# Optimization experiments

Hardware: AMD Instinct MI355X
Metric: run time of the kernel (lower is better)

## Reference

```python
import jax, jax.numpy as jnp
import numpy as np

ROPE_BASE = 10000.0

def apply_rope(x):
    # x: [B, S, H, Dh]  (rotate-half / NeoX convention)
    B, S, H, Dh = x.shape
    inv_freq = 1.0 / (ROPE_BASE ** (jnp.arange(0, Dh, 2, dtype=jnp.float32) / Dh))  # [Dh/2]
    ang = jnp.arange(S, dtype=jnp.float32)[:, None] * inv_freq[None, :]             # [S, Dh/2]
    cos = jnp.cos(ang)[None, :, None, :].astype(x.dtype)  # [1,S,1,Dh/2]
    sin = jnp.sin(ang)[None, :, None, :].astype(x.dtype)
    x1, x2 = jnp.split(x, 2, axis=-1)
    return jnp.concatenate([x1 * cos - x2 * sin, x1 * sin + x2 * cos], axis=-1)

def setup_inputs() -> dict:
    key = jax.random.key(0)
    k1, k2, k3 = jax.random.split(key, 3)
    B, S, D = 2, 2048, 1024
    x = jax.random.normal(k1, (B, S, D), dtype=jnp.float32)
    attn_mask = jnp.ones((B, S), dtype=bool)
    qkv_w = jax.random.normal(k2, (D, 3 * D), dtype=jnp.float32) * (1.0 / np.sqrt(D))
    out_w = jax.random.normal(k3, (D, D), dtype=jnp.float32) * (1.0 / np.sqrt(D))
    return {"x": x, "qkv_w": qkv_w, "out_w": out_w, "attn_mask": attn_mask, "is_causal": 1}

def reference(x, qkv_w, out_w, attn_mask, is_causal):
    B, S, D = x.shape
    H = 16
    Dh = D // H
    qkv = x @ qkv_w                                  # [B,S,3D]
    q, k, v = jnp.split(qkv, 3, axis=-1)
    q = apply_rope(q.reshape(B, S, H, Dh))           # [B,S,H,Dh]
    k = apply_rope(k.reshape(B, S, H, Dh))
    v = v.reshape(B, S, H, Dh)
    scale = 1.0 / np.sqrt(Dh)
    att = jnp.einsum('bqhd,bkhd->bhqk', q, k) * scale  # [B,H,S,S]
    if is_causal:
        mask = jnp.tril(jnp.ones((S, S), dtype=bool))[None, None]
    else:
        mask = attn_mask[:, None, None, :]             # [B,1,1,S]
    att = jnp.where(mask, att, jnp.finfo(att.dtype).min)
    p = jax.nn.softmax(att, axis=-1)
    y = jnp.einsum('bhqk,bkhd->bqhd', p, v).reshape(B, S, D)
    return y @ out_w
```

## Files before the change

kernel.cpp:

```cpp
#include <hip/hip_runtime.h>
#include <hip/hip_bf16.h>

#define BB 2
#define SS 2048
#define DD 1024
#define HH 16
#define N3 3072

#define POH (32 * 16 * 64 * 64)
#define PLH (32 * 16 * 64)

typedef __attribute__((ext_vector_type(8))) short bf16x8;
typedef __attribute__((ext_vector_type(4))) float f32x4;
typedef __attribute__((ext_vector_type(2))) unsigned int u32x2;

__device__ __forceinline__ float b2f(unsigned short u) {
    return __uint_as_float(((unsigned int)u) << 16);
}
__device__ __forceinline__ unsigned short f2b(float f) {
    unsigned int x = __float_as_uint(f);
    x += 0x7fffu + ((x >> 16) & 1u);
    return (unsigned short)(x >> 16);
}
__device__ __forceinline__ unsigned int pack2bf(float a, float b) {
    __hip_bfloat162 h = __float22bfloat162_rn(make_float2(a, b));
    return *(unsigned int*)&h;
}
__device__ __forceinline__ void storeC(float* p, float v) { *p = v; }
__device__ __forceinline__ void storeC(unsigned short* p, float v) { *p = f2b(v); }

__device__ __forceinline__ void gload_lds16(const void* g, void* l) {
    __builtin_amdgcn_global_load_lds(
        (__attribute__((address_space(1))) void*)g,
        (__attribute__((address_space(3))) void*)l, 16, 0, 0);
}

__global__ __launch_bounds__(256) void sincos_tab(float2* __restrict__ tab) {
    int i = blockIdx.x * 256 + threadIdx.x;
    int t = i & 31;
    int s = i >> 5;
    float inv = powf(10000.0f, -(float)t * (1.0f / 32.0f));
    float sn, c;
    sincosf((float)s * inv, &sn, &c);
    tab[i] = make_float2(c, sn);
}

__global__ __launch_bounds__(256) void cast_f32_bf16(
    const float* __restrict__ src, unsigned short* __restrict__ dst)
{
    int i = (blockIdx.x * 256 + threadIdx.x) * 4;
    float4 f = *(const float4*)(src + i);
    uint2 o;
    o.x = pack2bf(f.x, f.y);
    o.y = pack2bf(f.z, f.w);
    *(uint2*)(dst + i) = o;
}

__global__ __launch_bounds__(256) void cast_transpose(
    const float* __restrict__ src, unsigned short* __restrict__ dst,
    int R, int C)
{
    __shared__ unsigned short tile[64][66];
    const int t = threadIdx.x;
    const int c0 = blockIdx.x * 64, r0 = blockIdx.y * 64;
    const int lr = t >> 4;
    const int lc = (t & 15) * 4;
    #pragma unroll
    for (int i = 0; i < 4; ++i) {
        float4 f = *(const float4*)(src + (size_t)(r0 + lr + i * 16) * C + c0 + lc);
        tile[lr + i * 16][lc + 0] = f2b(f.x);
        tile[lr + i * 16][lc + 1] = f2b(f.y);
        tile[lr + i * 16][lc + 2] = f2b(f.z);
        tile[lr + i * 16][lc + 3] = f2b(f.w);
    }
    __syncthreads();
    #pragma unroll
    for (int i = 0; i < 4; ++i) {
        const int wr = lr + i * 16;
        ushort4 o;
        o.x = tile[lc + 0][wr];
        o.y = tile[lc + 1][wr];
        o.z = tile[lc + 2][wr];
        o.w = tile[lc + 3][wr];
        *(ushort4*)(dst + (size_t)(c0 + wr) * R + r0 + lc) = o;
    }
}

template <typename OutT, int TN>
__global__ __launch_bounds__(256) void gemm_mfma(
    const unsigned short* __restrict__ A,
    const unsigned short* __restrict__ Bt,
    OutT* __restrict__ C,
    int M, int N, int K)
{
    constexpr int NI = TN / 32;
    constexpr int NB = TN / 64;
    __shared__ unsigned short Al[128 * 32];
    __shared__ unsigned short Bl[TN * 32];
    const int tid  = threadIdx.x;
    const int wave = tid >> 6;
    const int lane = tid & 63;
    const int quad = lane >> 4;
    const int l16  = lane & 15;
    const int m0 = blockIdx.y * 128;
    const int n0 = blockIdx.x * TN;
    const int wm = (wave >> 1) * 64;
    const int wn = (wave & 1) * (TN / 2);

    const int srowA = wave * 32 + (lane >> 2);
    const int srowB = wave * (16 * NB) + (lane >> 2);
    const int scol  = (lane & 3) * 8;
    const unsigned short* gA = A  + (size_t)(m0 + srowA) * K + scol;
    const unsigned short* gB = Bt + (size_t)(n0 + srowB) * K + scol;

    f32x4 acc[4][NI];
    #pragma unroll
    for (int mi = 0; mi < 4; ++mi)
        #pragma unroll
        for (int ni = 0; ni < NI; ++ni)
            acc[mi][ni] = (f32x4){0.f, 0.f, 0.f, 0.f};

    for (int k0 = 0; k0 < K; k0 += 32) {
        __syncthreads();
        #pragma unroll
        for (int i = 0; i < 2; ++i)
            gload_lds16(gA + (size_t)i * 16 * K + k0, Al + (wave * 2 + i) * 512);
        #pragma unroll
        for (int i = 0; i < NB; ++i)
            gload_lds16(gB + (size_t)i * 16 * K + k0, Bl + (wave * NB + i) * 512);
        __syncthreads();

        bf16x8 af[4], bfr[NI];
        #pragma unroll
        for (int mi = 0; mi < 4; ++mi)
            af[mi] = *(const bf16x8*)&Al[(wm + mi * 16 + l16) * 32 + quad * 8];
        #pragma unroll
        for (int ni = 0; ni < NI; ++ni)
            bfr[ni] = *(const bf16x8*)&Bl[(wn + ni * 16 + l16) * 32 + quad * 8];
        #pragma unroll
        for (int mi = 0; mi < 4; ++mi)
            #pragma unroll
            for (int ni = 0; ni < NI; ++ni)
                acc[mi][ni] = __builtin_amdgcn_mfma_f32_16x16x32_bf16(
                    af[mi], bfr[ni], acc[mi][ni], 0, 0, 0);
    }

    #pragma unroll
    for (int mi = 0; mi < 4; ++mi) {
        #pragma unroll
        for (int r = 0; r < 4; ++r) {
            const size_t base = (size_t)(m0 + wm + mi * 16 + quad * 4 + r) * N + n0 + wn;
            #pragma unroll
            for (int ni = 0; ni < NI; ++ni)
                storeC(&C[base + ni * 16 + l16], acc[mi][ni][r]);
        }
    }
}

__global__ __launch_bounds__(256) void rope_split(
    const unsigned short* __restrict__ qkv,
    const float2* __restrict__ tab,
    unsigned short* __restrict__ qo,
    unsigned short* __restrict__ ko,
    unsigned short* __restrict__ vt)
{
    __shared__ unsigned short Vtile[64][72];

    const float SC = 0.18033688011112042f;
    const int s0 = blockIdx.x * 64;
    const int h  = blockIdx.y;
    const int b  = blockIdx.z;
    const int tid = threadIdx.x;
    const int sl = tid >> 2;
    const int qu = tid & 3;
    const size_t bh = (size_t)b * HH + h;

    const unsigned short* row = qkv + (size_t)(b * SS + s0 + sl) * N3 + h * 64;

    uint4 a0 = *(const uint4*)(row + qu * 8);
    uint4 a1 = *(const uint4*)(row + 32 + qu * 8);
    uint4 b0 = *(const uint4*)(row + DD + qu * 8);
    uint4 b1 = *(const uint4*)(row + DD + 32 + qu * 8);
    uint4 c0 = *(const uint4*)(row + 2 * DD + qu * 8);
    uint4 c1 = *(const uint4*)(row + 2 * DD + 32 + qu * 8);

    float2 cs[8];
    {
        const float4* tp = (const float4*)(tab + (size_t)(s0 + sl) * 32 + qu * 8);
        #pragma unroll
        for (int i = 0; i < 4; ++i) {
            float4 f = tp[i];
            cs[2 * i]     = make_float2(f.x, f.y);
            cs[2 * i + 1] = make_float2(f.z, f.w);
        }
    }

    const unsigned short* pa0 = (const unsigned short*)&a0;
    const unsigned short* pa1 = (const unsigned short*)&a1;
    const unsigned short* pb0 = (const unsigned short*)&b0;
    const unsigned short* pb1 = (const unsigned short*)&b1;
    const unsigned short* pc0 = (const unsigned short*)&c0;
    const unsigned short* pc1 = (const unsigned short*)&c1;

    unsigned short oq1[8], oq2[8], ok1[8], ok2[8];
    #pragma unroll
    for (int j = 0; j < 8; ++j) {
        float c = cs[j].x, sn = cs[j].y;
        float q1 = b2f(pa0[j]), q2 = b2f(pa1[j]);
        float k1 = b2f(pb0[j]), k2 = b2f(pb1[j]);
        oq1[j] = f2b((q1 * c - q2 * sn) * SC);
        oq2[j] = f2b((q1 * sn + q2 * c) * SC);
        ok1[j] = f2b(k1 * c - k2 * sn);
        ok2[j] = f2b(k1 * sn + k2 * c);
        Vtile[qu * 8 + j][sl]      = pc0[j];
        Vtile[32 + qu * 8 + j][sl] = pc1[j];
    }
    const size_t qoff = (bh * SS + s0 + sl) * 64;
    *(uint4*)(qo + qoff + qu * 8)      = *(const uint4*)oq1;
    *(uint4*)(qo + qoff + 32 + qu * 8) = *(const uint4*)oq2;
    *(uint4*)(ko + qoff + qu * 8)      = *(const uint4*)ok1;
    *(uint4*)(ko + qoff + 32 + qu * 8) = *(const uint4*)ok2;

    __syncthreads();

    const int dr = tid >> 2;
    const int ch = tid & 3;
    uint4 t0 = *(const uint4*)&Vtile[dr][ch * 16];
    uint4 t1 = *(const uint4*)&Vtile[dr][ch * 16 + 8];
    unsigned short* vrow = vt + (bh * 64 + dr) * SS + s0 + ch * 16;
    *(uint4*)vrow       = t0;
    *(uint4*)(vrow + 8) = t1;
}

__device__ __forceinline__ void attn_step(
    const unsigned short* __restrict__ Kb,
    const unsigned short* __restrict__ Vb,
    const bf16x8 qf0, const bf16x8 qf1, const bf16x8 onesf,
    f32x4 O[4], f32x4& l_acc,
    bool diag, const unsigned char* mrow,
    int kt, int quad, int l16, int csw, int qg)
{
    f32x4 Sf[4];
    __builtin_amdgcn_s_setprio(1);
    #pragma unroll
    for (int st = 0; st < 4; ++st) {
        const unsigned short* kr = &Kb[(st * 16 + l16) * 64];
        bf16x8 kf0 = *(const bf16x8*)(kr + csw * 8);
        bf16x8 kf1 = *(const bf16x8*)(kr + (csw ^ 4) * 8);
        f32x4 s = (f32x4){0.f, 0.f, 0.f, 0.f};
        s = __builtin_amdgcn_mfma_f32_16x16x32_bf16(kf0, qf0, s, 0, 0, 0);
        s = __builtin_amdgcn_mfma_f32_16x16x32_bf16(kf1, qf1, s, 0, 0, 0);
        Sf[st] = s;
    }
    __builtin_amdgcn_s_setprio(0);

    if (diag) {
        #pragma unroll
        for (int st = 0; st < 4; ++st) {
            const int kb0 = kt * 64 + st * 16 + quad * 4;
            #pragma unroll
            for (int r = 0; r < 4; ++r)
                if (kb0 + r > qg) Sf[st][r] = -1e30f;
        }
    } else if (mrow) {
        #pragma unroll
        for (int st = 0; st < 4; ++st) {
            uchar4 mv = *(const uchar4*)(mrow + st * 16 + quad * 4);
            if (!mv.x) Sf[st][0] = -1e30f;
            if (!mv.y) Sf[st][1] = -1e30f;
            if (!mv.z) Sf[st][2] = -1e30f;
            if (!mv.w) Sf[st][3] = -1e30f;
        }
    }

    #pragma unroll
    for (int st = 0; st < 4; ++st)
        #pragma unroll
        for (int r = 0; r < 4; ++r)
            Sf[st][r] = exp2f(Sf[st][r]);

    unsigned int W[4][2];
    #pragma unroll
    for (int st = 0; st < 4; ++st) {
        W[st][0] = pack2bf(Sf[st][0], Sf[st][1]);
        W[st][1] = pack2bf(Sf[st][2], Sf[st][3]);
    }

    unsigned int pw0[4], pw1[4];
    #pragma unroll
    for (int j = 0; j < 2; ++j) {
        u32x2 s1 = __builtin_amdgcn_permlane32_swap(W[0][j], W[1][j], false, false);
        u32x2 s2 = __builtin_amdgcn_permlane16_swap(s1.x, s1.y, false, false);
        pw0[j]     = s2.x;
        pw0[j + 2] = s2.y;
        u32x2 t1 = __builtin_amdgcn_permlane32_swap(W[2][j], W[3][j], false, false);
        u32x2 t2 = __builtin_amdgcn_permlane16_swap(t1.x, t1.y, false, false);
        pw1[j]     = t2.x;
        pw1[j + 2] = t2.y;
    }
    bf16x8 pf0 = *(const bf16x8*)pw0;
    bf16x8 pf1 = *(const bf16x8*)pw1;

    __builtin_amdgcn_s_setprio(1);
    l_acc = __builtin_amdgcn_mfma_f32_16x16x32_bf16(onesf, pf0, l_acc, 0, 0, 0);
    l_acc = __builtin_amdgcn_mfma_f32_16x16x32_bf16(onesf, pf1, l_acc, 0, 0, 0);
    #pragma unroll
    for (int st = 0; st < 4; ++st) {
        const unsigned short* vr = &Vb[(st * 16 + l16) * 64];
        bf16x8 vf0 = *(const bf16x8*)(vr + csw * 8);
        bf16x8 vf1 = *(const bf16x8*)(vr + (csw ^ 4) * 8);
        O[st] = __builtin_amdgcn_mfma_f32_16x16x32_bf16(vf0, pf0, O[st], 0, 0, 0);
        O[st] = __builtin_amdgcn_mfma_f32_16x16x32_bf16(vf1, pf1, O[st], 0, 0, 0);
    }
    __builtin_amdgcn_s_setprio(0);
}

__global__ __launch_bounds__(256) void flash_attn(
    const unsigned short* __restrict__ q,
    const unsigned short* __restrict__ k,
    const unsigned short* __restrict__ vt,
    unsigned short* __restrict__ y,
    float* __restrict__ pO,
    float* __restrict__ pL,
    const int* __restrict__ is_causal,
    const unsigned char* __restrict__ attn_mask)
{
    __shared__ unsigned short Kl[2][64 * 64];
    __shared__ unsigned short Vl[2][64 * 64];

    const int bid  = blockIdx.x;
    const int work = (bid & 7) * 192 + (bid >> 3);
    const int bhi  = work / 48;
    const int s    = work % 48;
    const int b = bhi >> 4;
    const int h = bhi & 15;
    const bool causal = (is_causal[0] != 0);

    int tile, k0t, k1t;
    bool split;
    if (s < 16) {
        tile = 16 + s; k0t = 0; k1t = 15; split = true;
    } else {
        const int r = s - 16, p = r >> 1;
        if (r & 1) { tile = 15 - p; k0t = 0;  k1t = causal ? tile : 31; split = false; }
        else       { tile = 31 - p; k0t = 16; k1t = causal ? tile : 31; split = true;  }
    }
    const int half = (s < 16) ? 0 : 1;

    const int tid  = threadIdx.x;
    const int wave = tid >> 6;
    const int lane = tid & 63;
    const int quad = lane >> 4;
    const int l16  = lane & 15;

    const size_t bh = (size_t)b * HH + h;

    const int qg = tile * 64 + wave * 16 + l16;
    const unsigned short* qrow = q + (bh * SS + qg) * 64;
    const bf16x8 qf0 = *(const bf16x8*)(qrow + quad * 8);
    const bf16x8 qf1 = *(const bf16x8*)(qrow + 32 + quad * 8);

    bf16x8 onesf;
    #pragma unroll
    for (int i = 0; i < 8; ++i) onesf[i] = (short)0x3F80;

    const unsigned short* kbase  = k  + bh * SS * 64;
    const unsigned short* vtbase = vt + bh * 64 * SS;

    const int Rl  = lane >> 3;
    const int cph = lane & 7;
    const int csw = quad ^ (l16 & 7);

    f32x4 O[4];
    #pragma unroll
    for (int st = 0; st < 4; ++st) O[st] = (f32x4){0.f, 0.f, 0.f, 0.f};
    f32x4 l_acc = (f32x4){0.f, 0.f, 0.f, 0.f};

    auto stage = [&](int kt) {
        const int buf = kt & 1;
        #pragma unroll
        for (int i = 0; i < 2; ++i) {
            const int jj = wave * 2 + i;
            const int R  = jj * 8 + Rl;
            const int cl = cph ^ (R & 7);
            gload_lds16(kbase + ((size_t)(kt * 64 + R) * 64 + cl * 8),
                        &Kl[buf][jj * 512]);
            gload_lds16(vtbase + ((size_t)R * SS + kt * 64 + cl * 8),
                        &Vl[buf][jj * 512]);
        }
    };

    stage(k0t);
    for (int kt = k0t; kt <= k1t; ++kt) {
        __syncthreads();
        if (kt + 1 <= k1t) stage(kt + 1);

        const unsigned char* mrow = causal ? nullptr
                                           : (attn_mask + (size_t)b * SS + kt * 64);
        attn_step(Kl[kt & 1], Vl[kt & 1], qf0, qf1, onesf, O, l_acc,
                  causal && kt == tile, mrow, kt, quad, l16, csw, qg);
    }

    if (!split) {
        const float inv = 1.0f / l_acc[0];
        unsigned short* yrow = y + ((size_t)b * SS + qg) * DD + h * 64;
        #pragma unroll
        for (int st = 0; st < 4; ++st) {
            uint2 o;
            o.x = pack2bf(O[st][0] * inv, O[st][1] * inv);
            o.y = pack2bf(O[st][2] * inv, O[st][3] * inv);
            *(uint2*)(yrow + st * 16 + quad * 4) = o;
        }
    } else {
        float* ob = pO + (size_t)half * POH
                  + (((bh * 16 + (size_t)(tile - 16)) * 64 + wave * 16 + l16) * 64);
        #pragma unroll
        for (int st = 0; st < 4; ++st)
            *(f32x4*)(ob + st * 16 + quad * 4) = O[st];
        if (quad == 0)
            pL[(size_t)half * PLH + (bh * 16 + (size_t)(tile - 16)) * 64
               + wave * 16 + l16] = l_acc[0];
    }
}

__global__ __launch_bounds__(256) void attn_merge(
    const float* __restrict__ pO, const float* __restrict__ pL,
    unsigned short* __restrict__ y)
{
    const int i = (blockIdx.x * 256 + threadIdx.x) * 4;
    float4 oa = *(const float4*)(pO + i);
    float4 obv = *(const float4*)(pO + POH + i);
    const int rowi = i >> 6;
    const int d    = i & 63;
    const float inv = 1.0f / (pL[rowi] + pL[PLH + rowi]);
    const int row = rowi & 63;
    const int tt  = (rowi >> 6) & 15;
    const int bh  = rowi >> 10;
    const int b = bh >> 4, h = bh & 15;
    const int sq = (16 + tt) * 64 + row;
    unsigned short* yp = y + ((size_t)b * SS + sq) * DD + h * 64 + d;
    uint2 ov;
    ov.x = pack2bf((oa.x + obv.x) * inv, (oa.y + obv.y) * inv);
    ov.y = pack2bf((oa.z + obv.z) * inv, (oa.w + obv.w) * inv);
    *(uint2*)yp = ov;
}

extern "C" void kernel_launch(void* const* d_in, const int* in_sizes, int n_in,
                              void* d_out, int out_size, void* d_ws, size_t ws_size,
                              hipStream_t stream) {
    const float* x      = (const float*)d_in[0];
    const float* qkv_w  = (const float*)d_in[1];
    const float* out_w  = (const float*)d_in[2];
    const unsigned char* mask = (const unsigned char*)d_in[3];
    const int*   is_c   = (const int*)d_in[4];
    float* out = (float*)d_out;

    unsigned short* xb  = (unsigned short*)d_ws;
    unsigned short* w1t = xb  + (size_t)4096 * 1024;
    unsigned short* w2t = w1t + (size_t)3072 * 1024;
    unsigned short* qkv = w2t + (size_t)1024 * 1024;
    unsigned short* qb  = qkv + (size_t)4096 * 3072;
    unsigned short* kb  = qb  + (size_t)BB * HH * SS * 64;
    unsigned short* vt  = kb  + (size_t)BB * HH * SS * 64;
    float2* tab = (float2*)(vt + (size_t)BB * HH * SS * 64);
    unsigned short* yb = xb;

    float* pO = (float*)qkv;
    float* pL = pO + (size_t)2 * POH;

    sincos_tab<<<(SS * 32) / 256, 256, 0, stream>>>(tab);
    cast_f32_bf16<<<(4096 * 1024) / 1024, 256, 0, stream>>>(x, xb);
    cast_transpose<<<dim3(N3 / 64, DD / 64), 256, 0, stream>>>(qkv_w, w1t, DD, N3);
    cast_transpose<<<dim3(DD / 64, DD / 64), 256, 0, stream>>>(out_w, w2t, DD, DD);

    gemm_mfma<unsigned short, 128><<<dim3(N3 / 128, 4096 / 128), 256, 0, stream>>>(
        xb, w1t, qkv, 4096, N3, DD);

    rope_split<<<dim3(SS / 64, HH, BB), 256, 0, stream>>>(qkv, tab, qb, kb, vt);

    flash_attn<<<dim3(48 * BB * HH), 256, 0, stream>>>(qb, kb, vt, yb, pO, pL,
                                                       is_c, mask);

    attn_merge<<<2048, 256, 0, stream>>>(pO, pL, yb);

    gemm_mfma<float, 64><<<dim3(DD / 64, 4096 / 128), 256, 0, stream>>>(
        yb, w2t, out, 4096, DD, DD);
}
```

Baseline: 210.6 us.

## Fuse RoPE, Q/K/V split and V transpose into QKV GEMM epilogue

The QKV projection GEMM now applies RoPE and the softmax scale to Q/K in its epilogue and writes Q, K and transposed V directly. This removes the separate rope_split kernel and the round trip of the full qkv intermediate through global memory. Each wave tile of 64 columns maps to exactly one head, so the rotate-half pairs sit in the same thread's accumulators. The epilogue stores are scattered 2-byte writes, and the V stores are strided 8-byte writes, which may be less coalesced. The output projection GEMM tile width also changes from 64 to 128.

Measured after the change: 218.4 us. +3.7%, slower.

```diff
diff --git a/kernel.cpp b/kernel.cpp
--- a/kernel.cpp
+++ b/kernel.cpp
@@ -157,79 +157,107 @@
     }
 }
 
-__global__ __launch_bounds__(256) void rope_split(
-    const unsigned short* __restrict__ qkv,
+__global__ __launch_bounds__(256) void gemm_qkv_rope(
+    const unsigned short* __restrict__ A,
+    const unsigned short* __restrict__ Bt,
     const float2* __restrict__ tab,
     unsigned short* __restrict__ qo,
     unsigned short* __restrict__ ko,
     unsigned short* __restrict__ vt)
 {
-    __shared__ unsigned short Vtile[64][72];
-
-    const float SC = 0.18033688011112042f;
-    const int s0 = blockIdx.x * 64;
-    const int h  = blockIdx.y;
-    const int b  = blockIdx.z;
-    const int tid = threadIdx.x;
-    const int sl = tid >> 2;
-    const int qu = tid & 3;
+    constexpr int K = DD;
+    __shared__ unsigned short Al[128 * 32];
+    __shared__ unsigned short Bl[128 * 32];
+    const int tid  = threadIdx.x;
+    const int wave = tid >> 6;
+    const int lane = tid & 63;
+    const int quad = lane >> 4;
+    const int l16  = lane & 15;
+    const int m0 = blockIdx.y * 128;
+    const int n0 = blockIdx.x * 128;
+    const int wm = (wave >> 1) * 64;
+    const int wn = (wave & 1) * 64;
+
+    const int srow = wave * 32 + (lane >> 2);
+    const int scol = (lane & 3) * 8;
+    const unsigned short* gA = A  + (size_t)(m0 + srow) * K + scol;
+    const unsigned short* gB = Bt + (size_t)(n0 + srow) * K + scol;
+
+    f32x4 acc[4][4];
+    #pragma unroll
+    for (int mi = 0; mi < 4; ++mi)
+        #pragma unroll
+        for (int ni = 0; ni < 4; ++ni)
+            acc[mi][ni] = (f32x4){0.f, 0.f, 0.f, 0.f};
+
+    for (int k0 = 0; k0 < K; k0 += 32) {
+        __syncthreads();
+        #pragma unroll
+        for (int i = 0; i < 2; ++i) {
+            gload_lds16(gA + (size_t)i * 16 * K + k0, Al + (wave * 2 + i) * 512);
+            gload_lds16(gB + (size_t)i * 16 * K + k0, Bl + (wave * 2 + i) * 512);
+        }
+        __syncthreads();
+
+        bf16x8 af[4], bfr[4];
+        #pragma unroll
+        for (int mi = 0; mi < 4; ++mi)
+            af[mi] = *(const bf16x8*)&Al[(wm + mi * 16 + l16) * 32 + quad * 8];
+        #pragma unroll
+        for (int ni = 0; ni < 4; ++ni)
+            bfr[ni] = *(const bf16x8*)&Bl[(wn + ni * 16 + l16) * 32 + quad * 8];
+        #pragma unroll
+        for (int mi = 0; mi < 4; ++mi)
+            #pragma unroll
+            for (int ni = 0; ni < 4; ++ni)
+                acc[mi][ni] = __builtin_amdgcn_mfma_f32_16x16x32_bf16(
+                    af[mi], bfr[ni], acc[mi][ni], 0, 0, 0);
+    }
+
+    const int gc  = n0 + wn;
+    const int sec = gc >> 10;
+    const int h   = (gc & 1023) >> 6;
+    const int s0g = m0 + wm;
+    const int b   = s0g >> 11;
     const size_t bh = (size_t)b * HH + h;
 
-    const unsigned short* row = qkv + (size_t)(b * SS + s0 + sl) * N3 + h * 64;
-
-    uint4 a0 = *(const uint4*)(row + qu * 8);
-    uint4 a1 = *(const uint4*)(row + 32 + qu * 8);
-    uint4 b0 = *(const uint4*)(row + DD + qu * 8);
-    uint4 b1 = *(const uint4*)(row + DD + 32 + qu * 8);
-    uint4 c0 = *(const uint4*)(row + 2 * DD + qu * 8);
-    uint4 c1 = *(const uint4*)(row + 2 * DD + 32 + qu * 8);
-
-    float2 cs[8];
-    {
-        const float4* tp = (const float4*)(tab + (size_t)(s0 + sl) * 32 + qu * 8);
-        #pragma unroll
-        for (int i = 0; i < 4; ++i) {
-            float4 f = tp[i];
-            cs[2 * i]     = make_float2(f.x, f.y);
-            cs[2 * i + 1] = make_float2(f.z, f.w);
-        }
-    }
-
-    const unsigned short* pa0 = (const unsigned short*)&a0;
-    const unsigned short* pa1 = (const unsigned short*)&a1;
-    const unsigned short* pb0 = (const unsigned short*)&b0;
-    const unsigned short* pb1 = (const unsigned short*)&b1;
-    const unsigned short* pc0 = (const unsigned short*)&c0;
-    const unsigned short* pc1 = (const unsigned short*)&c1;
-
-    unsigned short oq1[8], oq2[8], ok1[8], ok2[8];
-    #pragma unroll
-    for (int j = 0; j < 8; ++j) {
-        float c = cs[j].x, sn = cs[j].y;
-        float q1 = b2f(pa0[j]), q2 = b2f(pa1[j]);
-        float k1 = b2f(pb0[j]), k2 = b2f(pb1[j]);
-        oq1[j] = f2b((q1 * c - q2 * sn) * SC);
-        oq2[j] = f2b((q1 * sn + q2 * c) * SC);
-        ok1[j] = f2b(k1 * c - k2 * sn);
-        ok2[j] = f2b(k1 * sn + k2 * c);
-        Vtile[qu * 8 + j][sl]      = pc0[j];
-        Vtile[32 + qu * 8 + j][sl] = pc1[j];
-    }
-    const size_t qoff = (bh * SS + s0 + sl) * 64;
-    *(uint4*)(qo + qoff + qu * 8)      = *(const uint4*)oq1;
-    *(uint4*)(qo + qoff + 32 + qu * 8) = *(const uint4*)oq2;
-    *(uint4*)(ko + qoff + qu * 8)      = *(const uint4*)ok1;
-    *(uint4*)(ko + qoff + 32 + qu * 8) = *(const uint4*)ok2;
-
-    __syncthreads();
-
-    const int dr = tid >> 2;
-    const int ch = tid & 3;
-    uint4 t0 = *(const uint4*)&Vtile[dr][ch * 16];
-    uint4 t1 = *(const uint4*)&Vtile[dr][ch * 16 + 8];
-    unsigned short* vrow = vt + (bh * 64 + dr) * SS + s0 + ch * 16;
-    *(uint4*)vrow       = t0;
-    *(uint4*)(vrow + 8) = t1;
+    if (sec < 2) {
+        const float SCq = (sec == 0) ? 0.18033688011112042f : 1.0f;
+        unsigned short* dst = (sec == 0) ? qo : ko;
+        #pragma unroll
+        for (int mi = 0; mi < 4; ++mi) {
+            #pragma unroll
+            for (int r = 0; r < 4; ++r) {
+                const int ss = (s0g + mi * 16 + quad * 4 + r) & (SS - 1);
+                const float2* tp = tab + (size_t)ss * 32;
+                unsigned short* row = dst + (bh * SS + ss) * 64;
+                #pragma unroll
+                for (int ni = 0; ni < 2; ++ni) {
+                    const int t = ni * 16 + l16;
+                    float2 cs = tp[t];
+                    const float x1 = acc[mi][ni][r];
+                    const float x2 = acc[mi][ni + 2][r];
+                    row[t]      = f2b((x1 * cs.x - x2 * cs.y) * SCq);
+                    row[t + 32] = f2b((x1 * cs.y + x2 * cs.x) * SCq);
+                }
+            }
+        }
+    } else {
+        #pragma unroll
+        for (int mi = 0; mi < 4; ++mi) {
+            const int ss0 = (s0g + mi * 16 + quad * 4) & (SS - 1);
+            #pragma unroll
+            for (int ni = 0; ni < 4; ++ni) {
+                const int d = ni * 16 + l16;
+                ushort4 o;
+                o.x = f2b(acc[mi][ni][0]);
+                o.y = f2b(acc[mi][ni][1]);
+                o.z = f2b(acc[mi][ni][2]);
+                o.w = f2b(acc[mi][ni][3]);
+                *(ushort4*)(vt + (bh * 64 + d) * SS + ss0) = o;
+            }
+        }
+    }
 }
 
 __device__ __forceinline__ void attn_step(
@@ -473,16 +501,14 @@
     cast_transpose<<<dim3(N3 / 64, DD / 64), 256, 0, stream>>>(qkv_w, w1t, DD, N3);
     cast_transpose<<<dim3(DD / 64, DD / 64), 256, 0, stream>>>(out_w, w2t, DD, DD);
 
-    gemm_mfma<unsigned short, 128><<<dim3(N3 / 128, 4096 / 128), 256, 0, stream>>>(
-        xb, w1t, qkv, 4096, N3, DD);
-
-    rope_split<<<dim3(SS / 64, HH, BB), 256, 0, stream>>>(qkv, tab, qb, kb, vt);
+    gemm_qkv_rope<<<dim3(N3 / 128, 4096 / 128), 256, 0, stream>>>(
+        xb, w1t, tab, qb, kb, vt);
 
     flash_attn<<<dim3(48 * BB * HH), 256, 0, stream>>>(qb, kb, vt, yb, pO, pL,
                                                        is_c, mask);
 
     attn_merge<<<2048, 256, 0, stream>>>(pO, pL, yb);
 
-    gemm_mfma<float, 64><<<dim3(DD / 64, 4096 / 128), 256, 0, stream>>>(
+    gemm_mfma<float, 128><<<dim3(DD / 128, 4096 / 128), 256, 0, stream>>>(
         yb, w2t, out, 4096, DD, DD);
 }
```
